# Performance work log

Hardware: AMD Instinct MI355X
Metric: run time of the kernel (lower is better)

The kernel has to match this reference:

```python
import jax, jax.numpy as jnp
import numpy as np

D_MODEL = 2048
NUM_Q_HEADS = 32
NUM_KV_HEADS = 8
HEAD_DIM = D_MODEL // NUM_Q_HEADS  # 64
NUM_GROUPS = NUM_Q_HEADS // NUM_KV_HEADS  # 4


def setup_inputs() -> dict:
    key = jax.random.key(0)
    ks = jax.random.split(key, 9)
    s = 1.0 / np.sqrt(D_MODEL)
    x = jax.random.normal(ks[0], (2, 2048, D_MODEL), dtype=jnp.float32)
    Wq = jax.random.uniform(ks[1], (D_MODEL, NUM_Q_HEADS * HEAD_DIM), jnp.float32, -s, s)
    bq = jax.random.uniform(ks[2], (NUM_Q_HEADS * HEAD_DIM,), jnp.float32, -s, s)
    Wk = jax.random.uniform(ks[3], (D_MODEL, NUM_KV_HEADS * HEAD_DIM), jnp.float32, -s, s)
    bk = jax.random.uniform(ks[4], (NUM_KV_HEADS * HEAD_DIM,), jnp.float32, -s, s)
    Wv = jax.random.uniform(ks[5], (D_MODEL, NUM_KV_HEADS * HEAD_DIM), jnp.float32, -s, s)
    bv = jax.random.uniform(ks[6], (NUM_KV_HEADS * HEAD_DIM,), jnp.float32, -s, s)
    Wo = jax.random.uniform(ks[7], (D_MODEL, D_MODEL), jnp.float32, -s, s)
    bo = jax.random.uniform(ks[8], (D_MODEL,), jnp.float32, -s, s)
    return {"x": x, "Wq": Wq, "bq": bq, "Wk": Wk, "bk": bk,
            "Wv": Wv, "bv": bv, "Wo": Wo, "bo": bo}


def reference(x, Wq, bq, Wk, bk, Wv, bv, Wo, bo):
    B, T, C = x.shape
    Hkv, G, Dh = NUM_KV_HEADS, NUM_GROUPS, HEAD_DIM
    # projections
    q = (x @ Wq + bq).reshape(B, T, Hkv, G, Dh)   # group G query heads per kv head
    k = (x @ Wk + bk).reshape(B, T, Hkv, Dh)
    v = (x @ Wv + bv).reshape(B, T, Hkv, Dh)
    scale = 1.0 / np.sqrt(Dh).astype(np.float32)
    # scores: [B, Hkv, G, T, T] (kv head broadcast over its G query heads)
    scores = jnp.einsum('btkgd,bskd->bkgts', q, k) * scale
    attn = jax.nn.softmax(scores, axis=-1)
    out = jnp.einsum('bkgts,bskd->btkgd', attn, v).reshape(B, T, C)
    return out @ Wo + bo
```

## Files before the change

kernel.cpp:

```cpp
#include <hip/hip_runtime.h>
#include <cstdint>
#include <cstddef>
#include <math.h>

typedef uint16_t bf16;
typedef __attribute__((ext_vector_type(8))) __bf16 bf16x8;
typedef __attribute__((ext_vector_type(2))) float f32x2;
typedef __attribute__((ext_vector_type(4))) float f32x4;
typedef __attribute__((ext_vector_type(16))) float f32x16;

#define MFMA16(a,b,c) __builtin_amdgcn_mfma_f32_16x16x32_bf16((a),(b),(c),0,0,0)
#define MFMA32(a,b,c) __builtin_amdgcn_mfma_f32_32x32x16_bf16((a),(b),(c),0,0,0)

__device__ __forceinline__ uint16_t f2bf(float f){
  uint32_t u = __float_as_uint(f);
  return (uint16_t)((u + 0x7fffu + ((u >> 16) & 1u)) >> 16);
}
__device__ __forceinline__ uint32_t pk2(float lo, float hi){
  return (uint32_t)f2bf(lo) | ((uint32_t)f2bf(hi) << 16);
}

__device__ __forceinline__ void gload_lds16(const void* g, void* l){
  __builtin_amdgcn_global_load_lds((const __attribute__((address_space(1))) void*)g,
                                   (__attribute__((address_space(3))) void*)l, 16, 0, 0);
}

__global__ void k_convert(const float* __restrict__ in, bf16* __restrict__ out, int n){
  int i = (blockIdx.x * 256 + threadIdx.x) * 4;
  if (i >= n) return;
  float4 v = *reinterpret_cast<const float4*>(in + i);
  uint32_t lo = pk2(v.x, v.y);
  uint32_t hi = pk2(v.z, v.w);
  uint2 pkv = make_uint2(lo, hi);
  *reinterpret_cast<uint2*>(out + i) = pkv;
}

__global__ void k_transposeW(const float* __restrict__ in, bf16* __restrict__ out, int R, int C){
  __shared__ float tile[64][65];
  int c0 = blockIdx.x * 64, r0 = blockIdx.y * 64;
  int t = threadIdx.x;
  int fx = t & 15, fy = t >> 4;
  #pragma unroll
  for (int i = 0; i < 4; i++){
    int r = fy + i*16;
    float4 v = *reinterpret_cast<const float4*>(in + (size_t)(r0 + r)*C + c0 + fx*4);
    tile[r][fx*4+0] = v.x; tile[r][fx*4+1] = v.y;
    tile[r][fx*4+2] = v.z; tile[r][fx*4+3] = v.w;
  }
  __syncthreads();
  int gx = t & 7, gy = t >> 3;
  #pragma unroll
  for (int i = 0; i < 2; i++){
    int c = gy + i*32;
    int rr = gx*8;
    union { bf16 h[8]; uint4 u; } pk_;
    #pragma unroll
    for (int j = 0; j < 8; j++) pk_.h[j] = f2bf(tile[rr+j][c]);
    *reinterpret_cast<uint4*>(out + (size_t)(c0 + c)*R + r0 + rr) = pk_.u;
  }
}

__device__ __forceinline__ void gemm128_core(
    const bf16* __restrict__ Abase, const bf16* __restrict__ Btbase,
    int lda, int ldb, int K, bf16* As, bf16* Bs, f32x4 acc[4][4])
{
  const int tid = threadIdx.x;
  const int wid = tid >> 6, lane = tid & 63;
  const int wr = wid >> 1, wc = wid & 1;
  const int lr = lane & 15, lg = lane >> 4;
  const f32x4 vzero = {0.f, 0.f, 0.f, 0.f};

  #pragma unroll
  for (int m = 0; m < 4; m++)
    #pragma unroll
    for (int n = 0; n < 4; n++)
      acc[m][n] = vzero;

  int srcA[4], srcB[4], dOff[4];
  #pragma unroll
  for (int i = 0; i < 4; i++){
    int d = i*4096 + wid*1024 + lane*16;
    int row = d >> 7, sp = (d >> 4) & 7;
    int sl = sp ^ (row & 7);
    srcA[i] = row * lda + sl * 8;
    srcB[i] = row * ldb + sl * 8;
    dOff[i] = i*4096 + wid*1024;
  }

  for (int k0 = 0; k0 < K; k0 += 64){
    #pragma unroll
    for (int i = 0; i < 4; i++)
      gload_lds16(Abase + k0 + srcA[i], (char*)As + dOff[i]);
    #pragma unroll
    for (int i = 0; i < 4; i++)
      gload_lds16(Btbase + k0 + srcB[i], (char*)Bs + dOff[i]);
    __syncthreads();
    #pragma unroll
    for (int ks = 0; ks < 2; ks++){
      bf16x8 af[4], bfr[4];
      #pragma unroll
      for (int m = 0; m < 4; m++){
        int row = wr*64 + m*16 + lr;
        int sp = (ks*4 + lg) ^ (row & 7);
        af[m] = *reinterpret_cast<const bf16x8*>(As + row*64 + sp*8);
      }
      #pragma unroll
      for (int n = 0; n < 4; n++){
        int row = wc*64 + n*16 + lr;
        int sp = (ks*4 + lg) ^ (row & 7);
        bfr[n] = *reinterpret_cast<const bf16x8*>(Bs + row*64 + sp*8);
      }
      #pragma unroll
      for (int m = 0; m < 4; m++)
        #pragma unroll
        for (int n = 0; n < 4; n++)
          acc[m][n] = MFMA16(af[m], bfr[n], acc[m][n]);
    }
    __syncthreads();
  }
}

__global__ __launch_bounds__(256, 2) void k_qkv(
    const bf16* __restrict__ xb,
    const bf16* __restrict__ WqT, const bf16* __restrict__ WkT, const bf16* __restrict__ WvT,
    const float* __restrict__ bq, const float* __restrict__ bk, const float* __restrict__ bv,
    bf16* __restrict__ qo, bf16* __restrict__ ko, bf16* __restrict__ vtp)
{
  __shared__ __align__(16) bf16 As[128*64];
  __shared__ __align__(16) bf16 Bs[128*64];
  int by = blockIdx.y;
  const bf16* Bt; const float* bias; int mode; int y = 0; float scale = 1.f;
  if (by < 16){      Bt = WqT + (size_t)by*128*2048;      bias = bq + by*128; mode = 0; y = by;   scale = 0.18033688011112042f; }
  else if (by < 20){ y = by-16; Bt = WkT + (size_t)y*128*2048; bias = bk + y*128; mode = 1; }
  else {             y = by-20; Bt = WvT + (size_t)y*128*2048; bias = bv + y*128; mode = 2; }
  int m0 = blockIdx.x * 128;
  f32x4 acc[4][4];
  gemm128_core(xb + (size_t)m0*2048, Bt, 2048, 2048, 2048, As, Bs, acc);
  const int tid = threadIdx.x, wid = tid >> 6, lane = tid & 63;
  const int wr = wid >> 1, wc = wid & 1, lr = lane & 15, lg = lane >> 4;
  if (mode == 2){
    #pragma unroll
    for (int n = 0; n < 4; n++){
      int cl = wc*64 + n*16 + lr;
      float bb = bias[cl];
      #pragma unroll
      for (int m = 0; m < 4; m++){
        int row0 = m0 + wr*64 + m*16 + lg*4;
        int bi = row0 >> 11, tl = row0 & 2047;
        union { bf16 h[4]; uint2 u; } pk_;
        #pragma unroll
        for (int r = 0; r < 4; r++) pk_.h[r] = f2bf(acc[m][n][r] + bb);
        *reinterpret_cast<uint2*>(vtp + ((size_t)bi*512 + y*128 + cl)*2048 + tl) = pk_.u;
      }
    }
  } else {
    bf16* outp = (mode == 0) ? (qo + y*128) : (ko + y*128);
    int ldc = (mode == 0) ? 2048 : 512;
    #pragma unroll
    for (int n = 0; n < 4; n++){
      int col = wc*64 + n*16 + lr;
      float bb = bias[col];
      #pragma unroll
      for (int m = 0; m < 4; m++)
        #pragma unroll
        for (int r = 0; r < 4; r++){
          int row = m0 + wr*64 + m*16 + lg*4 + r;
          outp[(size_t)row*ldc + col] = f2bf((acc[m][n][r] + bb) * scale);
        }
    }
  }
}

__global__ __launch_bounds__(256, 2) void k_oproj(
    const bf16* __restrict__ ab, const bf16* __restrict__ WoT,
    const float* __restrict__ bo, float* __restrict__ outp)
{
  __shared__ __align__(16) bf16 As[128*64];
  __shared__ __align__(16) bf16 Bs[128*64];
  int m0 = blockIdx.x * 128, n0 = blockIdx.y * 128;
  f32x4 acc[4][4];
  gemm128_core(ab + (size_t)m0*2048, WoT + (size_t)n0*2048, 2048, 2048, 2048, As, Bs, acc);
  const int tid = threadIdx.x, wid = tid >> 6, lane = tid & 63;
  const int wr = wid >> 1, wc = wid & 1, lr = lane & 15, lg = lane >> 4;
  #pragma unroll
  for (int n = 0; n < 4; n++){
    int col = n0 + wc*64 + n*16 + lr;
    float bb = bo[col];
    #pragma unroll
    for (int m = 0; m < 4; m++)
      #pragma unroll
      for (int r = 0; r < 4; r++){
        int row = m0 + wr*64 + m*16 + lg*4 + r;
        outp[(size_t)row*2048 + col] = acc[m][n][r] + bb;
      }
  }
}

__global__ __launch_bounds__(512, 4) void k_flash(
    const bf16* __restrict__ q, const bf16* __restrict__ kmat,
    const bf16* __restrict__ vt, bf16* __restrict__ ao)
{
  __shared__ __align__(16) char lds[65536];
  const int tid = threadIdx.x;
  const int wid = tid >> 6, lane = tid & 63;
  const int l31 = lane & 31, hi = lane >> 5;
  const int bh = blockIdx.y;
  const int b = bh >> 5, hq = bh & 31, kvh = hq >> 2;
  const int qt = blockIdx.x;
  const int qrow0 = b*2048 + qt*256 + wid*32;

  bf16x8 qf[4];
  {
    const bf16* qrow = q + (size_t)(qrow0 + l31)*2048 + hq*64 + hi*8;
    #pragma unroll
    for (int t = 0; t < 4; t++)
      qf[t] = *reinterpret_cast<const bf16x8*>(qrow + t*16);
  }

  f32x16 oacc[2];
  #pragma unroll
  for (int n = 0; n < 2; n++)
    #pragma unroll
    for (int r = 0; r < 16; r++) oacc[n][r] = 0.f;
  f32x2 rp[4];
  #pragma unroll
  for (int j = 0; j < 4; j++){ rp[j][0] = 0.f; rp[j][1] = 0.f; }
  const f32x16 zv = {0.f,0.f,0.f,0.f,0.f,0.f,0.f,0.f,0.f,0.f,0.f,0.f,0.f,0.f,0.f,0.f};

  const int r7 = l31 & 7;
  int A[8];
  #pragma unroll
  for (int j = 0; j < 8; j++)
    A[j] = l31*128 + (((2*j + hi) ^ r7) << 4);

  const bf16* kbase = kmat + (size_t)b*2048*512 + kvh*64;
  const bf16* vbase = vt + ((size_t)b*512 + kvh*64)*2048;

  int kSrc[2], vSrc[2];
  const int dOf = wid*1024;
  #pragma unroll
  for (int i = 0; i < 2; i++){
    int kdb = i*8192 + tid*16;
    int krow = kdb >> 7, ksp = (kdb >> 4) & 7, ksl = ksp ^ (krow & 7);
    kSrc[i] = krow*512 + ksl*8;
    int o = tid*16;
    int vrow = o >> 7, vsp = (o >> 4) & 7, vsl = vsp ^ (vrow & 7);
    vSrc[i] = vrow*2048 + i*64 + vsl*8;
  }

  #define STAGE(buf, st_) do { \
    const bf16* kb_ = kbase + (size_t)(st_)*128*512; \
    const bf16* vb_ = vbase + (st_)*128; \
    gload_lds16(kb_ + kSrc[0], lds + (buf)*16384 + dOf); \
    gload_lds16(kb_ + kSrc[1], lds + (buf)*16384 + 8192 + dOf); \
    gload_lds16(vb_ + vSrc[0], lds + 32768 + (buf)*16384 + dOf); \
    gload_lds16(vb_ + vSrc[1], lds + 32768 + (buf)*16384 + 8192 + dOf); \
  } while(0)

  #define LDK(j, imm) (*reinterpret_cast<const bf16x8*>(lds + A[j] + (imm)))
  #define LDV(j, imm) (*reinterpret_cast<const bf16x8*>(lds + A[j] + 32768 + (imm)))

  STAGE(0, 0);
  __syncthreads();

  int cur = 0;
  for (int st = 0; st < 16; st++){
    if (st < 15) STAGE(cur^1, st+1);

    #pragma unroll
    for (int c = 0; c < 2; c++){
      f32x16 sc[2];
      __builtin_amdgcn_s_setprio(1);
      #pragma unroll
      for (int n = 0; n < 2; n++)
        sc[n] = MFMA32(LDK(0, c*8192 + n*4096), qf[0], zv);
      #pragma unroll
      for (int t = 1; t < 4; t++)
        #pragma unroll
        for (int n = 0; n < 2; n++)
          sc[n] = MFMA32(LDK(t, c*8192 + n*4096), qf[t], sc[n]);
      __builtin_amdgcn_s_setprio(0);

      uint32_t pw[2][8];
      #pragma unroll
      for (int n = 0; n < 2; n++)
        #pragma unroll
        for (int j = 0; j < 8; j++){
          float plo = __builtin_amdgcn_exp2f(sc[n][2*j]);
          float phi = __builtin_amdgcn_exp2f(sc[n][2*j+1]);
          f32x2 e; e[0] = plo; e[1] = phi;
          rp[j & 3] += e;
          asm("v_cvt_pk_bf16_f32 %0, %1, %2" : "=v"(pw[n][j]) : "v"(plo), "v"(phi));
        }
      #pragma unroll
      for (int n = 0; n < 2; n++)
        #pragma unroll
        for (int h = 0; h < 2; h++){
          asm volatile("v_permlane32_swap_b32 %0, %1" : "+v"(pw[n][h*4+0]), "+v"(pw[n][h*4+2]));
          asm volatile("v_permlane32_swap_b32 %0, %1" : "+v"(pw[n][h*4+1]), "+v"(pw[n][h*4+3]));
        }

      __builtin_amdgcn_s_setprio(1);
      #pragma unroll
      for (int kk = 0; kk < 4; kk++){
        int n = kk >> 1, h = kk & 1;
        union { uint32_t w[4]; bf16x8 v; } pa;
        pa.w[0] = pw[n][h*4+0]; pa.w[1] = pw[n][h*4+1];
        pa.w[2] = pw[n][h*4+2]; pa.w[3] = pw[n][h*4+3];
        #pragma unroll
        for (int nd = 0; nd < 2; nd++)
          oacc[nd] = MFMA32(pa.v, LDV(kk, c*8192 + nd*4096), oacc[nd]);
      }
      __builtin_amdgcn_s_setprio(0);
    }
    __syncthreads();
    #pragma unroll
    for (int j = 0; j < 8; j++) A[j] ^= 16384;
    cur ^= 1;
  }
  #undef STAGE
  #undef LDK
  #undef LDV

  float rs = (rp[0][0] + rp[0][1]) + (rp[1][0] + rp[1][1])
           + (rp[2][0] + rp[2][1]) + (rp[3][0] + rp[3][1]);
  float l = rs + __shfl_xor(rs, 32);
  float linv = 1.f / l;
  float lv[16];
  #pragma unroll
  for (int r = 0; r < 16; r++){
    int qi = (r & 3) + 8*(r >> 2) + 4*hi;
    lv[r] = __shfl(linv, qi);
  }
  #pragma unroll
  for (int nd = 0; nd < 2; nd++)
    #pragma unroll
    for (int r = 0; r < 16; r++){
      int qi = (r & 3) + 8*(r >> 2) + 4*hi;
      int row = qrow0 + qi;
      ao[(size_t)row*2048 + hq*64 + nd*32 + l31] = f2bf(oacc[nd][r] * lv[r]);
    }
}

extern "C" void kernel_launch(void* const* d_in, const int* in_sizes, int n_in,
                              void* d_out, int out_size, void* d_ws, size_t ws_size,
                              hipStream_t stream)
{
  const float* x  = (const float*)d_in[0];
  const float* Wq = (const float*)d_in[1];
  const float* bq = (const float*)d_in[2];
  const float* Wk = (const float*)d_in[3];
  const float* bk = (const float*)d_in[4];
  const float* Wv = (const float*)d_in[5];
  const float* bv = (const float*)d_in[6];
  const float* Wo = (const float*)d_in[7];
  const float* bo = (const float*)d_in[8];
  float* out = (float*)d_out;

  char* ws = (char*)d_ws;
  size_t off = 0;
  auto alloc = [&](size_t bytes){ char* p = ws + off; off += (bytes + 255) & ~(size_t)255; return p; };
  bf16* xb  = (bf16*)alloc(2*2048*2048*2);
  bf16* WqT = (bf16*)alloc(2048*2048*2);
  bf16* WkT = (bf16*)alloc(512*2048*2);
  bf16* WvT = (bf16*)alloc(512*2048*2);
  bf16* WoT = (bf16*)alloc(2048*2048*2);
  bf16* qb  = (bf16*)alloc(4096*2048*2);
  bf16* kb  = (bf16*)alloc((size_t)4096*512*2);
  bf16* vtb = (bf16*)alloc((size_t)4096*512*2);
  bf16* aob = xb;

  k_convert<<<8192, 256, 0, stream>>>(x, xb, 2*2048*2048);
  k_transposeW<<<dim3(32,32), 256, 0, stream>>>(Wq, WqT, 2048, 2048);
  k_transposeW<<<dim3(8,32),  256, 0, stream>>>(Wk, WkT, 2048, 512);
  k_transposeW<<<dim3(8,32),  256, 0, stream>>>(Wv, WvT, 2048, 512);
  k_transposeW<<<dim3(32,32), 256, 0, stream>>>(Wo, WoT, 2048, 2048);
  k_qkv<<<dim3(32,24), 256, 0, stream>>>(xb, WqT, WkT, WvT, bq, bk, bv, qb, kb, vtb);
  k_flash<<<dim3(8,64), 512, 0, stream>>>(qb, kb, vtb, aob);
  k_oproj<<<dim3(32,16), 256, 0, stream>>>(aob, WoT, bo, out);
}
```

Before: 195.0 us.

## Process two query row groups per wave in flash attention to reuse K/V fragments

Each wave now handles 64 query rows (two 32-row groups) instead of 32, so every K and V fragment read from LDS feeds two MFMAs. This halves the LDS traffic per unit of compute and halves the grid's redundant K/V staging. Launch bounds drop to 2 blocks per CU to make room for the doubled accumulators and Q fragments. The cost is higher register pressure, fewer resident waves and only 256 blocks, which may not fill the GPU well.

```diff
diff --git a/kernel.cpp b/kernel.cpp
--- a/kernel.cpp
+++ b/kernel.cpp
@@ -196,7 +196,7 @@
   }
 }
 
-__global__ __launch_bounds__(512, 4) void k_flash(
+__global__ __launch_bounds__(512, 2) void k_flash(
     const bf16* __restrict__ q, const bf16* __restrict__ kmat,
     const bf16* __restrict__ vt, bf16* __restrict__ ao)
 {
@@ -207,24 +207,26 @@
   const int bh = blockIdx.y;
   const int b = bh >> 5, hq = bh & 31, kvh = hq >> 2;
   const int qt = blockIdx.x;
-  const int qrow0 = b*2048 + qt*256 + wid*32;
-
-  bf16x8 qf[4];
-  {
-    const bf16* qrow = q + (size_t)(qrow0 + l31)*2048 + hq*64 + hi*8;
+  const int qrow0 = b*2048 + qt*512 + wid*64;
+
+  bf16x8 qf[2][4];
+  #pragma unroll
+  for (int g = 0; g < 2; g++){
+    const bf16* qrow = q + (size_t)(qrow0 + g*32 + l31)*2048 + hq*64 + hi*8;
     #pragma unroll
     for (int t = 0; t < 4; t++)
-      qf[t] = *reinterpret_cast<const bf16x8*>(qrow + t*16);
-  }
-
-  f32x16 oacc[2];
-  #pragma unroll
-  for (int n = 0; n < 2; n++)
-    #pragma unroll
-    for (int r = 0; r < 16; r++) oacc[n][r] = 0.f;
-  f32x2 rp[4];
-  #pragma unroll
-  for (int j = 0; j < 4; j++){ rp[j][0] = 0.f; rp[j][1] = 0.f; }
+      qf[g][t] = *reinterpret_cast<const bf16x8*>(qrow + t*16);
+  }
+
+  f32x16 oacc[2][2];
+  #pragma unroll
+  for (int g = 0; g < 2; g++)
+    #pragma unroll
+    for (int n = 0; n < 2; n++)
+      #pragma unroll
+      for (int r = 0; r < 16; r++) oacc[g][n][r] = 0.f;
+  float rsg[2][2];
+  rsg[0][0]=0.f; rsg[0][1]=0.f; rsg[1][0]=0.f; rsg[1][1]=0.f;
   const f32x16 zv = {0.f,0.f,0.f,0.f,0.f,0.f,0.f,0.f,0.f,0.f,0.f,0.f,0.f,0.f,0.f,0.f};
 
   const int r7 = l31 & 7;
@@ -263,83 +265,96 @@
   STAGE(0, 0);
   __syncthreads();
 
-  int cur = 0;
   for (int st = 0; st < 16; st++){
-    if (st < 15) STAGE(cur^1, st+1);
+    if (st < 15) STAGE((st & 1)^1, st+1);
 
     #pragma unroll
     for (int c = 0; c < 2; c++){
-      f32x16 sc[2];
+      f32x16 sc[2][2];
       __builtin_amdgcn_s_setprio(1);
       #pragma unroll
-      for (int n = 0; n < 2; n++)
-        sc[n] = MFMA32(LDK(0, c*8192 + n*4096), qf[0], zv);
-      #pragma unroll
-      for (int t = 1; t < 4; t++)
+      for (int t = 0; t < 4; t++){
+        bf16x8 af0 = LDK(t, c*8192);
+        bf16x8 af1 = LDK(t, c*8192 + 4096);
+        if (t == 0){
+          sc[0][0] = MFMA32(af0, qf[0][0], zv);
+          sc[1][0] = MFMA32(af0, qf[1][0], zv);
+          sc[0][1] = MFMA32(af1, qf[0][0], zv);
+          sc[1][1] = MFMA32(af1, qf[1][0], zv);
+        } else {
+          sc[0][0] = MFMA32(af0, qf[0][t], sc[0][0]);
+          sc[1][0] = MFMA32(af0, qf[1][t], sc[1][0]);
+          sc[0][1] = MFMA32(af1, qf[0][t], sc[0][1]);
+          sc[1][1] = MFMA32(af1, qf[1][t], sc[1][1]);
+        }
+      }
+      __builtin_amdgcn_s_setprio(0);
+
+      uint32_t pw[2][2][8];
+      #pragma unroll
+      for (int g = 0; g < 2; g++){
         #pragma unroll
         for (int n = 0; n < 2; n++)
-          sc[n] = MFMA32(LDK(t, c*8192 + n*4096), qf[t], sc[n]);
-      __builtin_amdgcn_s_setprio(0);
-
-      uint32_t pw[2][8];
-      #pragma unroll
-      for (int n = 0; n < 2; n++)
-        #pragma unroll
-        for (int j = 0; j < 8; j++){
-          float plo = __builtin_amdgcn_exp2f(sc[n][2*j]);
-          float phi = __builtin_amdgcn_exp2f(sc[n][2*j+1]);
-          f32x2 e; e[0] = plo; e[1] = phi;
-          rp[j & 3] += e;
-          asm("v_cvt_pk_bf16_f32 %0, %1, %2" : "=v"(pw[n][j]) : "v"(plo), "v"(phi));
-        }
-      #pragma unroll
-      for (int n = 0; n < 2; n++)
-        #pragma unroll
-        for (int h = 0; h < 2; h++){
-          asm volatile("v_permlane32_swap_b32 %0, %1" : "+v"(pw[n][h*4+0]), "+v"(pw[n][h*4+2]));
-          asm volatile("v_permlane32_swap_b32 %0, %1" : "+v"(pw[n][h*4+1]), "+v"(pw[n][h*4+3]));
-        }
+          #pragma unroll
+          for (int j = 0; j < 8; j++){
+            float plo = __builtin_amdgcn_exp2f(sc[g][n][2*j]);
+            float phi = __builtin_amdgcn_exp2f(sc[g][n][2*j+1]);
+            rsg[g][j & 1] += plo + phi;
+            asm("v_cvt_pk_bf16_f32 %0, %1, %2" : "=v"(pw[g][n][j]) : "v"(plo), "v"(phi));
+          }
+        #pragma unroll
+        for (int n = 0; n < 2; n++)
+          #pragma unroll
+          for (int h = 0; h < 2; h++){
+            asm volatile("v_permlane32_swap_b32 %0, %1" : "+v"(pw[g][n][h*4+0]), "+v"(pw[g][n][h*4+2]));
+            asm volatile("v_permlane32_swap_b32 %0, %1" : "+v"(pw[g][n][h*4+1]), "+v"(pw[g][n][h*4+3]));
+          }
+      }
 
       __builtin_amdgcn_s_setprio(1);
       #pragma unroll
       for (int kk = 0; kk < 4; kk++){
         int n = kk >> 1, h = kk & 1;
-        union { uint32_t w[4]; bf16x8 v; } pa;
-        pa.w[0] = pw[n][h*4+0]; pa.w[1] = pw[n][h*4+1];
-        pa.w[2] = pw[n][h*4+2]; pa.w[3] = pw[n][h*4+3];
-        #pragma unroll
-        for (int nd = 0; nd < 2; nd++)
-          oacc[nd] = MFMA32(pa.v, LDV(kk, c*8192 + nd*4096), oacc[nd]);
+        union { uint32_t w[4]; bf16x8 v; } pa0, pa1;
+        #pragma unroll
+        for (int w_ = 0; w_ < 4; w_++){ pa0.w[w_] = pw[0][n][h*4+w_]; pa1.w[w_] = pw[1][n][h*4+w_]; }
+        #pragma unroll
+        for (int nd = 0; nd < 2; nd++){
+          bf16x8 vf = LDV(kk, c*8192 + nd*4096);
+          oacc[0][nd] = MFMA32(pa0.v, vf, oacc[0][nd]);
+          oacc[1][nd] = MFMA32(pa1.v, vf, oacc[1][nd]);
+        }
       }
       __builtin_amdgcn_s_setprio(0);
     }
     __syncthreads();
     #pragma unroll
     for (int j = 0; j < 8; j++) A[j] ^= 16384;
-    cur ^= 1;
   }
   #undef STAGE
   #undef LDK
   #undef LDV
 
-  float rs = (rp[0][0] + rp[0][1]) + (rp[1][0] + rp[1][1])
-           + (rp[2][0] + rp[2][1]) + (rp[3][0] + rp[3][1]);
-  float l = rs + __shfl_xor(rs, 32);
-  float linv = 1.f / l;
-  float lv[16];
-  #pragma unroll
-  for (int r = 0; r < 16; r++){
-    int qi = (r & 3) + 8*(r >> 2) + 4*hi;
-    lv[r] = __shfl(linv, qi);
-  }
-  #pragma unroll
-  for (int nd = 0; nd < 2; nd++)
+  #pragma unroll
+  for (int g = 0; g < 2; g++){
+    float rs = rsg[g][0] + rsg[g][1];
+    float l = rs + __shfl_xor(rs, 32);
+    float linv = 1.f / l;
+    float lv[16];
     #pragma unroll
     for (int r = 0; r < 16; r++){
       int qi = (r & 3) + 8*(r >> 2) + 4*hi;
-      int row = qrow0 + qi;
-      ao[(size_t)row*2048 + hq*64 + nd*32 + l31] = f2bf(oacc[nd][r] * lv[r]);
-    }
+      lv[r] = __shfl(linv, qi);
+    }
+    #pragma unroll
+    for (int nd = 0; nd < 2; nd++)
+      #pragma unroll
+      for (int r = 0; r < 16; r++){
+        int qi = (r & 3) + 8*(r >> 2) + 4*hi;
+        int row = qrow0 + g*32 + qi;
+        ao[(size_t)row*2048 + hq*64 + nd*32 + l31] = f2bf(oacc[g][nd][r] * lv[r]);
+      }
+  }
 }
 
 extern "C" void kernel_launch(void* const* d_in, const int* in_sizes, int n_in,
@@ -376,6 +391,6 @@
   k_transposeW<<<dim3(8,32),  256, 0, stream>>>(Wv, WvT, 2048, 512);
   k_transposeW<<<dim3(32,32), 256, 0, stream>>>(Wo, WoT, 2048, 2048);
   k_qkv<<<dim3(32,24), 256, 0, stream>>>(xb, WqT, WkT, WvT, bq, bk, bv, qb, kb, vtb);
-  k_flash<<<dim3(8,64), 512, 0, stream>>>(qb, kb, vtb, aob);
+  k_flash<<<dim3(4,64), 512, 0, stream>>>(qb, kb, vtb, aob);
   k_oproj<<<dim3(32,16), 256, 0, stream>>>(aob, WoT, bo, out);
 }
```

Measured after the change: 193.0 us. Within noise of the previous version (-1.0%).
